# Kernel tuning notes

Hardware: AMD Instinct MI355X
Metric: run time of the kernel (lower is better)

The kernel has to match this reference:

```python
import jax, jax.numpy as jnp
import numpy as np

TEMPERATURE = 0.07
COS_EPS = 1e-8          # torch F.cosine_similarity eps
MASK_FILL = -9e15       # value used to mask the diagonal


def setup_inputs() -> dict:
    key = jax.random.key(0)
    k1, k2 = jax.random.split(key)
    B, D = 4096, 256
    z_i = jax.random.normal(k1, (B, D), dtype=jnp.float32)
    z_j = jax.random.normal(k2, (B, D), dtype=jnp.float32)
    return {"z_i": z_i, "z_j": z_j}


def reference(z_i, z_j):
    B = z_i.shape[0]
    z = jnp.concatenate([z_i, z_j], axis=0)                 # [2B, D]
    # cosine similarity = normalized-GEMM (same math as broadcasted version)
    norms = jnp.maximum(jnp.linalg.norm(z, axis=-1, keepdims=True), COS_EPS)
    zn = z / norms                                          # [2B, D]
    sim = zn @ zn.T                                         # [2B, 2B]
    # fused diagonal mask + temperature scale
    diag = jnp.eye(2 * B, dtype=bool)
    logits = jnp.where(diag, MASK_FILL, sim) / TEMPERATURE  # [2B, 2B]
    # positive pair labels: row k pairs with row (k+B) mod 2B
    labels = jnp.concatenate([jnp.arange(B, 2 * B), jnp.arange(0, B)])
    logp = jax.nn.log_softmax(logits, axis=-1)
    loss = -jnp.mean(jnp.take_along_axis(logp, labels[:, None], axis=-1))
    return loss
```

## Files before the change

kernel.cpp:

```cpp
#include <hip/hip_runtime.h>
#include <hip/hip_bf16.h>

#define B_ROWS 4096
#define TWOB   8192
#define DIM    256
#define INV_T  14.285714285714286f

#define BM 128
#define BN 128
#define NSTRIP 16
#define CT_PER_STRIP 4

typedef __bf16 bf16x8 __attribute__((ext_vector_type(8)));
typedef float  f32x4  __attribute__((ext_vector_type(4)));

__global__ __launch_bounds__(256) void normalize_k(const float* __restrict__ zi,
                                                   const float* __restrict__ zj,
                                                   unsigned short* __restrict__ zn,
                                                   float* __restrict__ loss_acc,
                                                   unsigned int* __restrict__ counter) {
    if (blockIdx.x == 0 && threadIdx.x == 0) {
        loss_acc[0] = 0.0f;
        counter[0]  = 0u;
    }
    int wave = threadIdx.x >> 6;
    int lane = threadIdx.x & 63;
    int row  = blockIdx.x * 4 + wave;
    const float* src = (row < B_ROWS) ? (zi + (size_t)row * DIM)
                                      : (zj + (size_t)(row - B_ROWS) * DIM);
    float4 v = reinterpret_cast<const float4*>(src)[lane];
    float ss = v.x * v.x + v.y * v.y + v.z * v.z + v.w * v.w;
#pragma unroll
    for (int off = 32; off >= 1; off >>= 1) ss += __shfl_xor(ss, off);
    float norm = sqrtf(ss);
    norm = fmaxf(norm, 1e-8f);
    float inv = 1.0f / norm;
    ushort4 o;
    o.x = __builtin_bit_cast(unsigned short, __float2bfloat16(v.x * inv));
    o.y = __builtin_bit_cast(unsigned short, __float2bfloat16(v.y * inv));
    o.z = __builtin_bit_cast(unsigned short, __float2bfloat16(v.z * inv));
    o.w = __builtin_bit_cast(unsigned short, __float2bfloat16(v.w * inv));
    reinterpret_cast<ushort4*>(zn)[(size_t)row * 64 + lane] = o;
}

__global__ __launch_bounds__(256) void ntxent_main(const unsigned short* __restrict__ znu,
                                                   float* __restrict__ pos,
                                                   float* __restrict__ strip_sums) {
    const __bf16* zn = (const __bf16*)znu;
    __shared__ __attribute__((aligned(16))) __bf16 As[BM * 32];
    __shared__ __attribute__((aligned(16))) __bf16 Bs[BN * 32];
    __shared__ float rowsumL[2][BM];

    const int tid  = threadIdx.x;
    const int wave = tid >> 6;
    const int lane = tid & 63;
    const int wr = wave >> 1, wc = wave & 1;
    const int quad = lane >> 4, lc = lane & 15;
    const int rt    = blockIdx.x;
    const int strip = blockIdx.y;
    const int row0  = rt * BM;
    const int posTile = (rt + 32) & 63;

    int stg_off[2];
#pragma unroll
    for (int t = 0; t < 2; ++t) {
        int c  = (wave * 2 + t) * 64 + lane;
        int m  = c >> 2;
        int kc = (c & 3) ^ ((m & 3) ^ ((m >> 2) & 3));
        stg_off[t] = m * DIM + kc * 8;
    }

    const int sw    = (lc & 3) ^ ((lc >> 2) & 3);
    const int aBase = (wr * 64 + lc) * 64 + ((quad ^ sw) * 16);
    const int bBase = (wc * 64 + lc) * 64 + ((quad ^ sw) * 16);

    f32x4 acc[4][4];
    float rsum[4][4];
#pragma unroll
    for (int mi = 0; mi < 4; ++mi)
#pragma unroll
        for (int r = 0; r < 4; ++r) rsum[mi][r] = 0.0f;

    for (int ct = 0; ct < CT_PER_STRIP; ++ct) {
        const int colTile = strip * CT_PER_STRIP + ct;
        const int col0 = colTile * BN;
#pragma unroll
        for (int mi = 0; mi < 4; ++mi)
#pragma unroll
            for (int ni = 0; ni < 4; ++ni) acc[mi][ni] = f32x4{0.f, 0.f, 0.f, 0.f};

        for (int kt = 0; kt < 8; ++kt) {
            const int k0 = kt * 32;
            __syncthreads();
#pragma unroll
            for (int t = 0; t < 2; ++t) {
                const int j = wave * 2 + t;
                const __bf16* ga = zn + row0 * DIM + k0 + stg_off[t];
                const __bf16* gb = zn + col0 * DIM + k0 + stg_off[t];
                __builtin_amdgcn_global_load_lds(
                    (const __attribute__((address_space(1))) void*)ga,
                    (__attribute__((address_space(3))) void*)((char*)As + j * 1024), 16, 0, 0);
                __builtin_amdgcn_global_load_lds(
                    (const __attribute__((address_space(1))) void*)gb,
                    (__attribute__((address_space(3))) void*)((char*)Bs + j * 1024), 16, 0, 0);
            }
            __syncthreads();

            bf16x8 af[4], bfr[4];
#pragma unroll
            for (int mi = 0; mi < 4; ++mi)
                af[mi] = *(const bf16x8*)((const char*)As + aBase + mi * 1024);
#pragma unroll
            for (int ni = 0; ni < 4; ++ni)
                bfr[ni] = *(const bf16x8*)((const char*)Bs + bBase + ni * 1024);
#pragma unroll
            for (int mi = 0; mi < 4; ++mi)
#pragma unroll
                for (int ni = 0; ni < 4; ++ni)
                    acc[mi][ni] = __builtin_amdgcn_mfma_f32_16x16x32_bf16(
                        af[mi], bfr[ni], acc[mi][ni], 0, 0, 0);
        }

        const bool special = (colTile == rt) || (colTile == posTile);
#pragma unroll
        for (int mi = 0; mi < 4; ++mi) {
#pragma unroll
            for (int ni = 0; ni < 4; ++ni) {
                f32x4 a = acc[mi][ni];
#pragma unroll
                for (int r = 0; r < 4; ++r) {
                    float logit = a[r] * INV_T;
                    float e = __expf(logit);
                    if (special) {
                        int gr = row0 + wr * 64 + mi * 16 + quad * 4 + r;
                        int gc = col0 + wc * 64 + ni * 16 + lc;
                        if (gc == ((gr + B_ROWS) & (TWOB - 1))) pos[gr] = logit;
                        if (gr == gc) e = 0.0f;
                    }
                    rsum[mi][r] += e;
                }
            }
        }
    }

#pragma unroll
    for (int mi = 0; mi < 4; ++mi) {
#pragma unroll
        for (int r = 0; r < 4; ++r) {
            float v = rsum[mi][r];
            v += __shfl_xor(v, 1);
            v += __shfl_xor(v, 2);
            v += __shfl_xor(v, 4);
            v += __shfl_xor(v, 8);
            if (lc == 0) rowsumL[wc][wr * 64 + mi * 16 + quad * 4 + r] = v;
        }
    }
    __syncthreads();
    if (tid < BM)
        strip_sums[(size_t)strip * TWOB + row0 + tid] = rowsumL[0][tid] + rowsumL[1][tid];
}

__global__ __launch_bounds__(256) void finalize_k(const float* __restrict__ strip_sums,
                                                  const float* __restrict__ pos,
                                                  float* __restrict__ loss_acc,
                                                  unsigned int* __restrict__ counter,
                                                  float* __restrict__ out) {
    __shared__ float wsums[4];
    const int tid = threadIdx.x;
    const int r   = blockIdx.x * 256 + tid;
    float s = 0.0f;
#pragma unroll
    for (int st = 0; st < NSTRIP; ++st) s += strip_sums[(size_t)st * TWOB + r];
    float local = logf(s) - pos[r];
#pragma unroll
    for (int off = 32; off >= 1; off >>= 1) local += __shfl_xor(local, off);
    if ((tid & 63) == 0) wsums[tid >> 6] = local;
    __syncthreads();
    if (tid == 0) {
        float bsum = wsums[0] + wsums[1] + wsums[2] + wsums[3];
        atomicAdd(loss_acc, bsum);
        __threadfence();
        unsigned int done = atomicAdd(counter, 1u);
        if (done == gridDim.x - 1) {
            float total = atomicAdd(loss_acc, 0.0f);
            out[0] = total / (float)TWOB;
        }
    }
}

extern "C" void kernel_launch(void* const* d_in, const int* in_sizes, int n_in,
                              void* d_out, int out_size, void* d_ws, size_t ws_size,
                              hipStream_t stream) {
    const float* zi = (const float*)d_in[0];
    const float* zj = (const float*)d_in[1];
    unsigned short* zn = (unsigned short*)d_ws;
    float* pos        = (float*)((char*)d_ws + (size_t)TWOB * DIM * 2);
    float* strip_sums = pos + TWOB;
    float* loss_acc   = strip_sums + (size_t)NSTRIP * TWOB;
    unsigned int* counter = (unsigned int*)(loss_acc + 1);
    float* out = (float*)d_out;

    normalize_k<<<dim3(TWOB / 4), 256, 0, stream>>>(zi, zj, zn, loss_acc, counter);
    ntxent_main<<<dim3(64, NSTRIP), 256, 0, stream>>>(zn, pos, strip_sums);
    finalize_k<<<dim3(TWOB / 256), 256, 0, stream>>>(strip_sums, pos, loss_acc, counter, out);
}
```

Measured before the change: 115.6 us.

## Double-buffer LDS tiles to overlap global-to-LDS loads with MFMA compute

The A and B LDS tiles become two buffers each, and the column-tile and k loops are flattened into one 32-step loop. The next k-slice is issued with global_load_lds into the spare buffer right after a single barrier, so it can overlap with the MFMAs on the current buffer. This removes one of the two barriers per k step and hides global load latency. In exchange the kernel uses twice as much LDS, which may lower occupancy, and the per-tile epilogue is now placed inside the flattened loop.

```diff
diff --git a/kernel.cpp b/kernel.cpp
--- a/kernel.cpp
+++ b/kernel.cpp
@@ -10,6 +10,7 @@
 #define BN 128
 #define NSTRIP 16
 #define CT_PER_STRIP 4
+#define NIT (CT_PER_STRIP * 8)
 
 typedef __bf16 bf16x8 __attribute__((ext_vector_type(8)));
 typedef float  f32x4  __attribute__((ext_vector_type(4)));
@@ -47,8 +48,8 @@
                                                    float* __restrict__ pos,
                                                    float* __restrict__ strip_sums) {
     const __bf16* zn = (const __bf16*)znu;
-    __shared__ __attribute__((aligned(16))) __bf16 As[BM * 32];
-    __shared__ __attribute__((aligned(16))) __bf16 Bs[BN * 32];
+    __shared__ __attribute__((aligned(16))) __bf16 As[2][BM * 32];
+    __shared__ __attribute__((aligned(16))) __bf16 Bs[2][BN * 32];
     __shared__ float rowsumL[2][BM];
 
     const int tid  = threadIdx.x;
@@ -74,6 +75,25 @@
     const int aBase = (wr * 64 + lc) * 64 + ((quad ^ sw) * 16);
     const int bBase = (wc * 64 + lc) * 64 + ((quad ^ sw) * 16);
 
+    auto stage = [&](int it, int buf) {
+        const int kt   = it & 7;
+        const int ct   = it >> 3;
+        const int col0 = (strip * CT_PER_STRIP + ct) * BN;
+        const int k0   = kt * 32;
+#pragma unroll
+        for (int t = 0; t < 2; ++t) {
+            const int j = wave * 2 + t;
+            const __bf16* ga = zn + row0 * DIM + k0 + stg_off[t];
+            const __bf16* gb = zn + col0 * DIM + k0 + stg_off[t];
+            __builtin_amdgcn_global_load_lds(
+                (const __attribute__((address_space(1))) void*)ga,
+                (__attribute__((address_space(3))) void*)((char*)As + buf * 8192 + j * 1024), 16, 0, 0);
+            __builtin_amdgcn_global_load_lds(
+                (const __attribute__((address_space(1))) void*)gb,
+                (__attribute__((address_space(3))) void*)((char*)Bs + buf * 8192 + j * 1024), 16, 0, 0);
+        }
+    };
+
     f32x4 acc[4][4];
     float rsum[4][4];
 #pragma unroll
@@ -81,63 +101,55 @@
 #pragma unroll
         for (int r = 0; r < 4; ++r) rsum[mi][r] = 0.0f;
 
-    for (int ct = 0; ct < CT_PER_STRIP; ++ct) {
-        const int colTile = strip * CT_PER_STRIP + ct;
-        const int col0 = colTile * BN;
+    stage(0, 0);
+
+    for (int it = 0; it < NIT; ++it) {
+        const int buf = it & 1;
+        if ((it & 7) == 0) {
+#pragma unroll
+            for (int mi = 0; mi < 4; ++mi)
+#pragma unroll
+                for (int ni = 0; ni < 4; ++ni) acc[mi][ni] = f32x4{0.f, 0.f, 0.f, 0.f};
+        }
+
+        __syncthreads();
+        if (it + 1 < NIT) stage(it + 1, buf ^ 1);
+
+        bf16x8 af[4], bfr[4];
 #pragma unroll
         for (int mi = 0; mi < 4; ++mi)
-#pragma unroll
-            for (int ni = 0; ni < 4; ++ni) acc[mi][ni] = f32x4{0.f, 0.f, 0.f, 0.f};
-
-        for (int kt = 0; kt < 8; ++kt) {
-            const int k0 = kt * 32;
-            __syncthreads();
-#pragma unroll
-            for (int t = 0; t < 2; ++t) {
-                const int j = wave * 2 + t;
-                const __bf16* ga = zn + row0 * DIM + k0 + stg_off[t];
-                const __bf16* gb = zn + col0 * DIM + k0 + stg_off[t];
-                __builtin_amdgcn_global_load_lds(
-                    (const __attribute__((address_space(1))) void*)ga,
-                    (__attribute__((address_space(3))) void*)((char*)As + j * 1024), 16, 0, 0);
-                __builtin_amdgcn_global_load_lds(
-                    (const __attribute__((address_space(1))) void*)gb,
-                    (__attribute__((address_space(3))) void*)((char*)Bs + j * 1024), 16, 0, 0);
-            }
-            __syncthreads();
-
-            bf16x8 af[4], bfr[4];
-#pragma unroll
-            for (int mi = 0; mi < 4; ++mi)
-                af[mi] = *(const bf16x8*)((const char*)As + aBase + mi * 1024);
+            af[mi] = *(const bf16x8*)((const char*)As + buf * 8192 + aBase + mi * 1024);
+#pragma unroll
+        for (int ni = 0; ni < 4; ++ni)
+            bfr[ni] = *(const bf16x8*)((const char*)Bs + buf * 8192 + bBase + ni * 1024);
+#pragma unroll
+        for (int mi = 0; mi < 4; ++mi)
 #pragma unroll
             for (int ni = 0; ni < 4; ++ni)
-                bfr[ni] = *(const bf16x8*)((const char*)Bs + bBase + ni * 1024);
-#pragma unroll
-            for (int mi = 0; mi < 4; ++mi)
-#pragma unroll
-                for (int ni = 0; ni < 4; ++ni)
-                    acc[mi][ni] = __builtin_amdgcn_mfma_f32_16x16x32_bf16(
-                        af[mi], bfr[ni], acc[mi][ni], 0, 0, 0);
-        }
-
-        const bool special = (colTile == rt) || (colTile == posTile);
-#pragma unroll
-        for (int mi = 0; mi < 4; ++mi) {
-#pragma unroll
-            for (int ni = 0; ni < 4; ++ni) {
-                f32x4 a = acc[mi][ni];
-#pragma unroll
-                for (int r = 0; r < 4; ++r) {
-                    float logit = a[r] * INV_T;
-                    float e = __expf(logit);
-                    if (special) {
-                        int gr = row0 + wr * 64 + mi * 16 + quad * 4 + r;
-                        int gc = col0 + wc * 64 + ni * 16 + lc;
-                        if (gc == ((gr + B_ROWS) & (TWOB - 1))) pos[gr] = logit;
-                        if (gr == gc) e = 0.0f;
+                acc[mi][ni] = __builtin_amdgcn_mfma_f32_16x16x32_bf16(
+                    af[mi], bfr[ni], acc[mi][ni], 0, 0, 0);
+
+        if ((it & 7) == 7) {
+            const int colTile = strip * CT_PER_STRIP + (it >> 3);
+            const int col0 = colTile * BN;
+            const bool special = (colTile == rt) || (colTile == posTile);
+#pragma unroll
+            for (int mi = 0; mi < 4; ++mi) {
+#pragma unroll
+                for (int ni = 0; ni < 4; ++ni) {
+                    f32x4 a = acc[mi][ni];
+#pragma unroll
+                    for (int r = 0; r < 4; ++r) {
+                        float logit = a[r] * INV_T;
+                        float e = __expf(logit);
+                        if (special) {
+                            int gr = row0 + wr * 64 + mi * 16 + quad * 4 + r;
+                            int gc = col0 + wc * 64 + ni * 16 + lc;
+                            if (gc == ((gr + B_ROWS) & (TWOB - 1))) pos[gr] = logit;
+                            if (gr == gc) e = 0.0f;
+                        }
+                        rsum[mi][r] += e;
                     }
-                    rsum[mi][r] += e;
                 }
             }
         }
```

Measured after the change: 155.2 us. 34.3% more time.

## Keep the A row tile resident in LDS and double-buffer B tiles across strips

Applied to the files above, without the earlier changes.

Each block now preloads its full 128x256 A row tile into LDS once and reuses it for every column tile in the strip, instead of reloading A on every k-step. B tiles are double-buffered, with the next k-slice prefetched right after a single barrier, which removes one __syncthreads per k-step. Strips are halved to 8, each covering 8 column tiles, so there are fewer blocks and fewer partial sums to write out. The cost is about 80KB of LDS per block, which limits occupancy, and overlap depends on how the compiler places vmcnt waits for the async LDS loads.

```diff
diff --git a/kernel.cpp b/kernel.cpp
--- a/kernel.cpp
+++ b/kernel.cpp
@@ -8,8 +8,8 @@
 
 #define BM 128
 #define BN 128
-#define NSTRIP 16
-#define CT_PER_STRIP 4
+#define NSTRIP 8
+#define CT_PER_STRIP 8
 
 typedef __bf16 bf16x8 __attribute__((ext_vector_type(8)));
 typedef float  f32x4  __attribute__((ext_vector_type(4)));
@@ -47,9 +47,8 @@
                                                    float* __restrict__ pos,
                                                    float* __restrict__ strip_sums) {
     const __bf16* zn = (const __bf16*)znu;
-    __shared__ __attribute__((aligned(16))) __bf16 As[BM * 32];
-    __shared__ __attribute__((aligned(16))) __bf16 Bs[BN * 32];
-    __shared__ float rowsumL[2][BM];
+    __shared__ __attribute__((aligned(16))) __bf16 As[8][BM * 32];
+    __shared__ __attribute__((aligned(16))) __bf16 Bs[2][BN * 32];
 
     const int tid  = threadIdx.x;
     const int wave = tid >> 6;
@@ -74,6 +73,29 @@
     const int aBase = (wr * 64 + lc) * 64 + ((quad ^ sw) * 16);
     const int bBase = (wc * 64 + lc) * 64 + ((quad ^ sw) * 16);
 
+#pragma unroll
+    for (int kt = 0; kt < 8; ++kt) {
+#pragma unroll
+        for (int t = 0; t < 2; ++t) {
+            const int j = wave * 2 + t;
+            const __bf16* ga = zn + row0 * DIM + kt * 32 + stg_off[t];
+            __builtin_amdgcn_global_load_lds(
+                (const __attribute__((address_space(1))) void*)ga,
+                (__attribute__((address_space(3))) void*)((char*)As + kt * 8192 + j * 1024), 16, 0, 0);
+        }
+    }
+    {
+        const int col0 = strip * CT_PER_STRIP * BN;
+#pragma unroll
+        for (int t = 0; t < 2; ++t) {
+            const int j = wave * 2 + t;
+            const __bf16* gb = zn + col0 * DIM + stg_off[t];
+            __builtin_amdgcn_global_load_lds(
+                (const __attribute__((address_space(1))) void*)gb,
+                (__attribute__((address_space(3))) void*)((char*)Bs + j * 1024), 16, 0, 0);
+        }
+    }
+
     f32x4 acc[4][4];
     float rsum[4][4];
 #pragma unroll
@@ -89,30 +111,34 @@
 #pragma unroll
             for (int ni = 0; ni < 4; ++ni) acc[mi][ni] = f32x4{0.f, 0.f, 0.f, 0.f};
 
+#pragma unroll
         for (int kt = 0; kt < 8; ++kt) {
-            const int k0 = kt * 32;
             __syncthreads();
-#pragma unroll
-            for (int t = 0; t < 2; ++t) {
-                const int j = wave * 2 + t;
-                const __bf16* ga = zn + row0 * DIM + k0 + stg_off[t];
-                const __bf16* gb = zn + col0 * DIM + k0 + stg_off[t];
-                __builtin_amdgcn_global_load_lds(
-                    (const __attribute__((address_space(1))) void*)ga,
-                    (__attribute__((address_space(3))) void*)((char*)As + j * 1024), 16, 0, 0);
-                __builtin_amdgcn_global_load_lds(
-                    (const __attribute__((address_space(1))) void*)gb,
-                    (__attribute__((address_space(3))) void*)((char*)Bs + j * 1024), 16, 0, 0);
+
+            {
+                const int nct = (kt == 7) ? ct + 1 : ct;
+                const int nkt = (kt + 1) & 7;
+                if (nct < CT_PER_STRIP) {
+                    const int ncol0 = (strip * CT_PER_STRIP + nct) * BN;
+#pragma unroll
+                    for (int t = 0; t < 2; ++t) {
+                        const int j = wave * 2 + t;
+                        const __bf16* gb = zn + ncol0 * DIM + nkt * 32 + stg_off[t];
+                        __builtin_amdgcn_global_load_lds(
+                            (const __attribute__((address_space(1))) void*)gb,
+                            (__attribute__((address_space(3))) void*)((char*)Bs + ((kt + 1) & 1) * 8192 + j * 1024),
+                            16, 0, 0);
+                    }
+                }
             }
-            __syncthreads();
 
             bf16x8 af[4], bfr[4];
 #pragma unroll
             for (int mi = 0; mi < 4; ++mi)
-                af[mi] = *(const bf16x8*)((const char*)As + aBase + mi * 1024);
+                af[mi] = *(const bf16x8*)((const char*)As + kt * 8192 + aBase + mi * 1024);
 #pragma unroll
             for (int ni = 0; ni < 4; ++ni)
-                bfr[ni] = *(const bf16x8*)((const char*)Bs + bBase + ni * 1024);
+                bfr[ni] = *(const bf16x8*)((const char*)Bs + (kt & 1) * 8192 + bBase + ni * 1024);
 #pragma unroll
             for (int mi = 0; mi < 4; ++mi)
 #pragma unroll
@@ -143,6 +169,8 @@
         }
     }
 
+    __syncthreads();
+    float* rowsumL = (float*)As;
 #pragma unroll
     for (int mi = 0; mi < 4; ++mi) {
 #pragma unroll
@@ -152,12 +180,12 @@
             v += __shfl_xor(v, 2);
             v += __shfl_xor(v, 4);
             v += __shfl_xor(v, 8);
-            if (lc == 0) rowsumL[wc][wr * 64 + mi * 16 + quad * 4 + r] = v;
+            if (lc == 0) rowsumL[wc * BM + wr * 64 + mi * 16 + quad * 4 + r] = v;
         }
     }
     __syncthreads();
     if (tid < BM)
-        strip_sums[(size_t)strip * TWOB + row0 + tid] = rowsumL[0][tid] + rowsumL[1][tid];
+        strip_sums[(size_t)strip * TWOB + row0 + tid] = rowsumL[tid] + rowsumL[BM + tid];
 }
 
 __global__ __launch_bounds__(256) void finalize_k(const float* __restrict__ strip_sums,
```

Result: faster. 107.2 us (-7.2%).

## Load MFMA fragments directly from global with register double-buffering, drop LDS staging

Applied to the files above, without the earlier changes.

Replaces the LDS-staged tile loads and their two barriers per k-step with direct per-lane global loads of bf16x8 fragments, prefetching the next k-step into registers while the current MFMAs run. It also folds the temperature scale into an exp2 multiplier. This removes barrier and LDS overhead, but waves sharing a tile no longer share data through LDS, so global/L2 traffic rises and register pressure grows.

```diff
diff --git a/kernel.cpp b/kernel.cpp
--- a/kernel.cpp
+++ b/kernel.cpp
@@ -5,6 +5,7 @@
 #define TWOB   8192
 #define DIM    256
 #define INV_T  14.285714285714286f
+#define EXPSCALE 20.609865074705232f
 
 #define BM 128
 #define BN 128
@@ -46,9 +47,7 @@
 __global__ __launch_bounds__(256) void ntxent_main(const unsigned short* __restrict__ znu,
                                                    float* __restrict__ pos,
                                                    float* __restrict__ strip_sums) {
-    const __bf16* zn = (const __bf16*)znu;
-    __shared__ __attribute__((aligned(16))) __bf16 As[BM * 32];
-    __shared__ __attribute__((aligned(16))) __bf16 Bs[BN * 32];
+    const bf16x8* __restrict__ znv = (const bf16x8*)znu;
     __shared__ float rowsumL[2][BM];
 
     const int tid  = threadIdx.x;
@@ -61,18 +60,15 @@
     const int row0  = rt * BM;
     const int posTile = (rt + 32) & 63;
 
-    int stg_off[2];
-#pragma unroll
-    for (int t = 0; t < 2; ++t) {
-        int c  = (wave * 2 + t) * 64 + lane;
-        int m  = c >> 2;
-        int kc = (c & 3) ^ ((m & 3) ^ ((m >> 2) & 3));
-        stg_off[t] = m * DIM + kc * 8;
-    }
-
-    const int sw    = (lc & 3) ^ ((lc >> 2) & 3);
-    const int aBase = (wr * 64 + lc) * 64 + ((quad ^ sw) * 16);
-    const int bBase = (wc * 64 + lc) * 64 + ((quad ^ sw) * 16);
+    const int arow = row0 + wr * 64 + lc;
+    int aidx[4], bidx[4];
+#pragma unroll
+    for (int mi = 0; mi < 4; ++mi) aidx[mi] = (arow + mi * 16) * 32 + quad;
+    {
+        const int brow = strip * CT_PER_STRIP * BN + wc * 64 + lc;
+#pragma unroll
+        for (int ni = 0; ni < 4; ++ni) bidx[ni] = (brow + ni * 16) * 32 + quad;
+    }
 
     f32x4 acc[4][4];
     float rsum[4][4];
@@ -80,6 +76,12 @@
     for (int mi = 0; mi < 4; ++mi)
 #pragma unroll
         for (int r = 0; r < 4; ++r) rsum[mi][r] = 0.0f;
+
+    bf16x8 a_cur[4], b_cur[4];
+#pragma unroll
+    for (int mi = 0; mi < 4; ++mi) a_cur[mi] = znv[aidx[mi]];
+#pragma unroll
+    for (int ni = 0; ni < 4; ++ni) b_cur[ni] = znv[bidx[ni]];
 
     for (int ct = 0; ct < CT_PER_STRIP; ++ct) {
         const int colTile = strip * CT_PER_STRIP + ct;
@@ -89,36 +91,35 @@
 #pragma unroll
             for (int ni = 0; ni < 4; ++ni) acc[mi][ni] = f32x4{0.f, 0.f, 0.f, 0.f};
 
+#pragma unroll
         for (int kt = 0; kt < 8; ++kt) {
-            const int k0 = kt * 32;
-            __syncthreads();
-#pragma unroll
-            for (int t = 0; t < 2; ++t) {
-                const int j = wave * 2 + t;
-                const __bf16* ga = zn + row0 * DIM + k0 + stg_off[t];
-                const __bf16* gb = zn + col0 * DIM + k0 + stg_off[t];
-                __builtin_amdgcn_global_load_lds(
-                    (const __attribute__((address_space(1))) void*)ga,
-                    (__attribute__((address_space(3))) void*)((char*)As + j * 1024), 16, 0, 0);
-                __builtin_amdgcn_global_load_lds(
-                    (const __attribute__((address_space(1))) void*)gb,
-                    (__attribute__((address_space(3))) void*)((char*)Bs + j * 1024), 16, 0, 0);
+            bf16x8 a_nxt[4], b_nxt[4];
+            if (kt < 7) {
+#pragma unroll
+                for (int mi = 0; mi < 4; ++mi)
+                    a_nxt[mi] = znv[aidx[mi] + (kt + 1) * 4];
+#pragma unroll
+                for (int ni = 0; ni < 4; ++ni)
+                    b_nxt[ni] = znv[bidx[ni] + (kt + 1) * 4];
+            } else {
+                const int badd = (ct < CT_PER_STRIP - 1) ? BN * 32 : 0;
+#pragma unroll
+                for (int mi = 0; mi < 4; ++mi)
+                    a_nxt[mi] = znv[aidx[mi]];
+#pragma unroll
+                for (int ni = 0; ni < 4; ++ni) {
+                    bidx[ni] += badd;
+                    b_nxt[ni] = znv[bidx[ni]];
+                }
             }
-            __syncthreads();
-
-            bf16x8 af[4], bfr[4];
-#pragma unroll
-            for (int mi = 0; mi < 4; ++mi)
-                af[mi] = *(const bf16x8*)((const char*)As + aBase + mi * 1024);
-#pragma unroll
-            for (int ni = 0; ni < 4; ++ni)
-                bfr[ni] = *(const bf16x8*)((const char*)Bs + bBase + ni * 1024);
 #pragma unroll
             for (int mi = 0; mi < 4; ++mi)
 #pragma unroll
                 for (int ni = 0; ni < 4; ++ni)
                     acc[mi][ni] = __builtin_amdgcn_mfma_f32_16x16x32_bf16(
-                        af[mi], bfr[ni], acc[mi][ni], 0, 0, 0);
+                        a_cur[mi], b_cur[ni], acc[mi][ni], 0, 0, 0);
+#pragma unroll
+            for (int x = 0; x < 4; ++x) { a_cur[x] = a_nxt[x]; b_cur[x] = b_nxt[x]; }
         }
 
         const bool special = (colTile == rt) || (colTile == posTile);
@@ -129,12 +130,11 @@
                 f32x4 a = acc[mi][ni];
 #pragma unroll
                 for (int r = 0; r < 4; ++r) {
-                    float logit = a[r] * INV_T;
-                    float e = __expf(logit);
+                    float e = exp2f(a[r] * EXPSCALE);
                     if (special) {
                         int gr = row0 + wr * 64 + mi * 16 + quad * 4 + r;
                         int gc = col0 + wc * 64 + ni * 16 + lc;
-                        if (gc == ((gr + B_ROWS) & (TWOB - 1))) pos[gr] = logit;
+                        if (gc == ((gr + B_ROWS) & (TWOB - 1))) pos[gr] = a[r] * INV_T;
                         if (gr == gc) e = 0.0f;
                     }
                     rsum[mi][r] += e;
```

Measured after the change: 168.3 us. 1.46x slower.
